# Kernel optimization log

Hardware: AMD Instinct MI355X
Metric: run time of the kernel (lower is better)

The kernel has to match this reference:

```python
import jax, jax.numpy as jnp
import numpy as np

B, C, FS, Z_DIM, OUT_C, F_SIZE = 256, 512, 16, 64, 1, 3
NZ = FS * FS  # 256


def setup_inputs() -> dict:
    key = jax.random.key(0)
    k1, k2, k3, k4, k5 = jax.random.split(key, 5)
    # z: [B, C, H, W]
    z = jax.random.normal(k1, (B, C, FS, FS), dtype=jnp.float32)
    # 512 independent per-channel Linear(Nz -> z_dim): stacked weights/biases
    lim_in = 1.0 / np.sqrt(NZ)
    W_in = jax.random.uniform(k2, (C, NZ, Z_DIM), minval=-lim_in, maxval=lim_in, dtype=jnp.float32)
    b_in = jax.random.uniform(k3, (C, Z_DIM), minval=-lim_in, maxval=lim_in, dtype=jnp.float32)
    # shared Linear(z_dim -> out_channels*f_size*f_size)
    lim_out = 1.0 / np.sqrt(Z_DIM)
    W_out = jax.random.uniform(k4, (Z_DIM, OUT_C * F_SIZE * F_SIZE), minval=-lim_out, maxval=lim_out, dtype=jnp.float32)
    b_out = jax.random.uniform(k5, (OUT_C * F_SIZE * F_SIZE,), minval=-lim_out, maxval=lim_out, dtype=jnp.float32)
    return {"z": z, "W_in": W_in, "b_in": b_in, "W_out": W_out, "b_out": b_out}


def reference(z, W_in, b_in, W_out, b_out):
    batch = z.shape[0]
    # flatten each channel's HxW map: [B, C, Nz]
    x = z.reshape(batch, C, NZ)
    # per-channel Linear as one batched GEMM: [B, C, z_dim]
    a = jnp.einsum('bcn,cnz->bcz', x, W_in) + b_in[None, :, :]
    # shared output Linear: [B, C, out_c*f*f]
    k = jnp.einsum('bcz,zk->bck', a, W_out) + b_out
    # [B, C, out_channels, f_size, f_size]
    return k.reshape(batch, C, OUT_C, F_SIZE, F_SIZE)
```

## Files before the change

### kernel.cpp

```cpp
#include <hip/hip_runtime.h>

#define BB 256
#define CC 512
#define NZ 256
#define ZD 64
#define KK 9
#define WFSZ (KK * NZ)

template<int CTRL>
__device__ __forceinline__ float dpp_add(float v) {
    int o = __builtin_amdgcn_update_dpp(0, __float_as_int(v), CTRL, 0xF, 0xF, true);
    return v + __int_as_float(o);
}
__device__ __forceinline__ float red8(float v) {
    v = dpp_add<0xB1>(v);
    v = dpp_add<0x4E>(v);
    v = dpp_add<0x141>(v);
    return v;
}

__global__ __launch_bounds__(512, 2)
void wf_kernel(const float* __restrict__ W_in, const float* __restrict__ b_in,
               const float* __restrict__ W_out, const float* __restrict__ b_out,
               float* __restrict__ wf, float* __restrict__ biask) {
    __shared__ __align__(16) float s_woutT[KK * ZD];
    __shared__ float s_bin[ZD];
    const int c = blockIdx.x;
    const int t = threadIdx.x;

    for (int i = t; i < KK * ZD; i += 512) {
        float v = W_out[i];
        int zz = i / KK, k = i - zz * KK;
        s_woutT[k * ZD + zz] = v;
    }
    if (t < ZD) s_bin[t] = b_in[c * ZD + t];
    __syncthreads();

    const int n = t >> 1, half = t & 1;
    const float* wrow = W_in + ((size_t)c * NZ + n) * ZD + half * 32;
    float acc[KK];
#pragma unroll
    for (int k = 0; k < KK; ++k) acc[k] = 0.f;
#pragma unroll
    for (int j = 0; j < 8; ++j) {
        const float4 w = *reinterpret_cast<const float4*>(wrow + 4 * j);
#pragma unroll
        for (int k = 0; k < KK; ++k) {
            const float4 wo = *reinterpret_cast<const float4*>(
                &s_woutT[k * ZD + half * 32 + 4 * j]);
            acc[k] += w.x * wo.x + w.y * wo.y + w.z * wo.z + w.w * wo.w;
        }
    }
#pragma unroll
    for (int k = 0; k < KK; ++k) acc[k] = dpp_add<0xB1>(acc[k]);
    if (half == 0) {
#pragma unroll
        for (int k = 0; k < KK; ++k)
            wf[(size_t)c * WFSZ + k * NZ + n] = acc[k];
    }
    if (t < KK) {
        float s = 0.f;
        for (int zz = 0; zz < ZD; ++zz) s += s_bin[zz] * s_woutT[t * ZD + zz];
        biask[c * KK + t] = s + b_out[t];
    }
}

__global__ __launch_bounds__(256, 2)
void out_kernel(const float* __restrict__ z, const float* __restrict__ wf,
                const float* __restrict__ biask, float* __restrict__ out) {
    __shared__ __align__(16) float s_wf[WFSZ];
    __shared__ float s_bias[KK];

    const int cid = blockIdx.x & (CC - 1);
    const int chunk = blockIdx.x >> 9;
    const int t = threadIdx.x;
    const int lane = t & 63;
    const int wave = t >> 6;
    const int g = lane >> 3;
    const int sub = lane & 7;
    const int b0 = chunk * 64 + wave * 16 + g * 2;

    const size_t bstr = (size_t)CC * NZ;
    const float* xp = z + ((size_t)b0 * CC + cid) * NZ + sub * 4;
    float4 x0[8], x1[8];
#pragma unroll
    for (int j = 0; j < 8; ++j)
        x0[j] = *reinterpret_cast<const float4*>(xp + j * 32);
#pragma unroll
    for (int j = 0; j < 8; ++j)
        x1[j] = *reinterpret_cast<const float4*>(xp + bstr + j * 32);

    {
        const float4* wfg = reinterpret_cast<const float4*>(wf + (size_t)cid * WFSZ);
        float4* s4 = reinterpret_cast<float4*>(s_wf);
        for (int i = t; i < WFSZ / 4; i += 256) s4[i] = wfg[i];
        if (t < KK) s_bias[t] = biask[cid * KK + t];
    }
    __syncthreads();

    float a0[KK], a1[KK];
#pragma unroll
    for (int k = 0; k < KK; ++k) { a0[k] = 0.f; a1[k] = 0.f; }
#pragma unroll
    for (int k = 0; k < KK; ++k) {
#pragma unroll
        for (int j = 0; j < 8; ++j) {
            const float4 wfv = *reinterpret_cast<const float4*>(
                &s_wf[k * NZ + sub * 4 + j * 32]);
            a0[k] += x0[j].x * wfv.x + x0[j].y * wfv.y + x0[j].z * wfv.z + x0[j].w * wfv.w;
            a1[k] += x1[j].x * wfv.x + x1[j].y * wfv.y + x1[j].z * wfv.z + x1[j].w * wfv.w;
        }
    }
#pragma unroll
    for (int k = 0; k < KK; ++k) { a0[k] = red8(a0[k]); a1[k] = red8(a1[k]); }

    const float biasS = s_bias[sub];
    float v0 = a0[0], v1 = a1[0];
#pragma unroll
    for (int k = 1; k < 8; ++k) {
        if (sub == k) { v0 = a0[k]; v1 = a1[k]; }
    }
    const size_t o0 = ((size_t)b0 * CC + cid) * KK;
    const size_t o1 = o0 + (size_t)CC * KK;
    out[o0 + sub] = v0 + biasS;
    out[o1 + sub] = v1 + biasS;
    if (sub == 0) {
        out[o0 + 8] = a0[8] + s_bias[8];
        out[o1 + 8] = a1[8] + s_bias[8];
    }
}

extern "C" void kernel_launch(void* const* d_in, const int* in_sizes, int n_in,
                              void* d_out, int out_size, void* d_ws, size_t ws_size,
                              hipStream_t stream) {
    const float* z     = (const float*)d_in[0];
    const float* W_in  = (const float*)d_in[1];
    const float* b_in  = (const float*)d_in[2];
    const float* W_out = (const float*)d_in[3];
    const float* b_out = (const float*)d_in[4];
    float* out = (float*)d_out;

    float* wf    = (float*)d_ws;
    float* biask = (float*)d_ws + (size_t)CC * WFSZ;

    wf_kernel<<<dim3(CC), dim3(512), 0, stream>>>(W_in, b_in, W_out, b_out, wf, biask);
    out_kernel<<<dim3(4 * CC), dim3(256), 0, stream>>>(z, wf, biask, out);
}
```

Before: 233.9 us.

## Stream z through double-buffered LDS tiles, one block per channel

The output kernel now launches one block per channel instead of four batch chunks per channel. Each block loops over the batch in tiles of 32 rows and prefetches the next z tile into a second LDS buffer with asynchronous global-to-LDS loads while the current tile is being computed. The fused weight slice is loaded into LDS once per channel instead of four times, and the reduction widens to 16 lanes. In exchange the grid shrinks to 512 blocks with about 73KB of LDS each, which lowers parallelism. Correctness also depends on the async LDS loads having completed before each barrier.

Measured after the change: 228.8 us. -2.2%, faster.

```diff
diff --git a/kernel.cpp b/kernel.cpp
--- a/kernel.cpp
+++ b/kernel.cpp
@@ -6,17 +6,27 @@
 #define ZD 64
 #define KK 9
 #define WFSZ (KK * NZ)
+#define TR 32
+#define NT (BB / TR)
 
 template<int CTRL>
 __device__ __forceinline__ float dpp_add(float v) {
     int o = __builtin_amdgcn_update_dpp(0, __float_as_int(v), CTRL, 0xF, 0xF, true);
     return v + __int_as_float(o);
 }
-__device__ __forceinline__ float red8(float v) {
+__device__ __forceinline__ float red16(float v) {
     v = dpp_add<0xB1>(v);
     v = dpp_add<0x4E>(v);
     v = dpp_add<0x141>(v);
+    v = dpp_add<0x140>(v);
     return v;
+}
+
+__device__ __forceinline__ void gld_lds16(const float* g, float* l) {
+    __builtin_amdgcn_global_load_lds(
+        (const __attribute__((address_space(1))) unsigned int*)(g),
+        (__attribute__((address_space(3))) unsigned int*)(l),
+        16, 0, 0);
 }
 
 __global__ __launch_bounds__(512, 2)
@@ -68,65 +78,78 @@
 __global__ __launch_bounds__(256, 2)
 void out_kernel(const float* __restrict__ z, const float* __restrict__ wf,
                 const float* __restrict__ biask, float* __restrict__ out) {
+    __shared__ __align__(16) float s_z[2][TR * NZ];
     __shared__ __align__(16) float s_wf[WFSZ];
-    __shared__ float s_bias[KK];
+    __shared__ float s_b[KK];
 
-    const int cid = blockIdx.x & (CC - 1);
-    const int chunk = blockIdx.x >> 9;
+    const int c = blockIdx.x;
     const int t = threadIdx.x;
     const int lane = t & 63;
     const int wave = t >> 6;
-    const int g = lane >> 3;
-    const int sub = lane & 7;
-    const int b0 = chunk * 64 + wave * 16 + g * 2;
+    const int g16 = lane >> 4;
+    const int s16 = lane & 15;
 
-    const size_t bstr = (size_t)CC * NZ;
-    const float* xp = z + ((size_t)b0 * CC + cid) * NZ + sub * 4;
-    float4 x0[8], x1[8];
+    const size_t zrow = (size_t)CC * NZ;
+    const float* zc = z + (size_t)c * NZ;
+
 #pragma unroll
-    for (int j = 0; j < 8; ++j)
-        x0[j] = *reinterpret_cast<const float4*>(xp + j * 32);
-#pragma unroll
-    for (int j = 0; j < 8; ++j)
-        x1[j] = *reinterpret_cast<const float4*>(xp + bstr + j * 32);
+    for (int r = 0; r < 8; ++r)
+        gld_lds16(zc + (size_t)(wave * 8 + r) * zrow + lane * 4,
+                  &s_z[0][(wave * 8 + r) * NZ]);
 
     {
-        const float4* wfg = reinterpret_cast<const float4*>(wf + (size_t)cid * WFSZ);
+        const float4* g4 = reinterpret_cast<const float4*>(wf + (size_t)c * WFSZ);
         float4* s4 = reinterpret_cast<float4*>(s_wf);
-        for (int i = t; i < WFSZ / 4; i += 256) s4[i] = wfg[i];
-        if (t < KK) s_bias[t] = biask[cid * KK + t];
+        for (int i = t; i < WFSZ / 4; i += 256) s4[i] = g4[i];
+        if (t < KK) s_b[t] = biask[c * KK + t];
     }
-    __syncthreads();
 
-    float a0[KK], a1[KK];
+    const int r0 = wave * 8 + g16 * 2;
+
+#pragma unroll 1
+    for (int tl = 0; tl < NT; ++tl) {
+        __syncthreads();
+        const int cur = tl & 1;
+        if (tl + 1 < NT) {
+            const float* g0 = zc + (size_t)((tl + 1) * TR + wave * 8) * zrow;
 #pragma unroll
-    for (int k = 0; k < KK; ++k) { a0[k] = 0.f; a1[k] = 0.f; }
+            for (int r = 0; r < 8; ++r)
+                gld_lds16(g0 + (size_t)r * zrow + lane * 4,
+                          &s_z[cur ^ 1][(wave * 8 + r) * NZ]);
+        }
+
+        float a0[KK], a1[KK];
 #pragma unroll
-    for (int k = 0; k < KK; ++k) {
+        for (int k = 0; k < KK; ++k) { a0[k] = 0.f; a1[k] = 0.f; }
 #pragma unroll
-        for (int j = 0; j < 8; ++j) {
-            const float4 wfv = *reinterpret_cast<const float4*>(
-                &s_wf[k * NZ + sub * 4 + j * 32]);
-            a0[k] += x0[j].x * wfv.x + x0[j].y * wfv.y + x0[j].z * wfv.z + x0[j].w * wfv.w;
-            a1[k] += x1[j].x * wfv.x + x1[j].y * wfv.y + x1[j].z * wfv.z + x1[j].w * wfv.w;
+        for (int j = 0; j < 4; ++j) {
+            const float4 x0 = *reinterpret_cast<const float4*>(
+                &s_z[cur][r0 * NZ + j * 64 + s16 * 4]);
+            const float4 x1 = *reinterpret_cast<const float4*>(
+                &s_z[cur][(r0 + 1) * NZ + j * 64 + s16 * 4]);
+#pragma unroll
+            for (int k = 0; k < KK; ++k) {
+                const float4 w = *reinterpret_cast<const float4*>(
+                    &s_wf[k * NZ + j * 64 + s16 * 4]);
+                a0[k] += x0.x * w.x + x0.y * w.y + x0.z * w.z + x0.w * w.w;
+                a1[k] += x1.x * w.x + x1.y * w.y + x1.z * w.z + x1.w * w.w;
+            }
         }
-    }
 #pragma unroll
-    for (int k = 0; k < KK; ++k) { a0[k] = red8(a0[k]); a1[k] = red8(a1[k]); }
+        for (int k = 0; k < KK; ++k) { a0[k] = red16(a0[k]); a1[k] = red16(a1[k]); }
 
-    const float biasS = s_bias[sub];
-    float v0 = a0[0], v1 = a1[0];
+        float v0 = a0[0], v1 = a1[0];
 #pragma unroll
-    for (int k = 1; k < 8; ++k) {
-        if (sub == k) { v0 = a0[k]; v1 = a1[k]; }
-    }
-    const size_t o0 = ((size_t)b0 * CC + cid) * KK;
-    const size_t o1 = o0 + (size_t)CC * KK;
-    out[o0 + sub] = v0 + biasS;
-    out[o1 + sub] = v1 + biasS;
-    if (sub == 0) {
-        out[o0 + 8] = a0[8] + s_bias[8];
-        out[o1 + 8] = a1[8] + s_bias[8];
+        for (int k = 1; k < KK; ++k) {
+            if (s16 == k) { v0 = a0[k]; v1 = a1[k]; }
+        }
+        if (s16 < KK) {
+            const float bk = s_b[s16];
+            const int b = tl * TR + r0;
+            const size_t o0 = ((size_t)b * CC + c) * KK;
+            out[o0 + s16] = v0 + bk;
+            out[o0 + (size_t)CC * KK + s16] = v1 + bk;
+        }
     }
 }
 
@@ -140,9 +163,9 @@
     const float* b_out = (const float*)d_in[4];
     float* out = (float*)d_out;
 
-    float* wf    = (float*)d_ws;
+    float* wfbuf = (float*)d_ws;
     float* biask = (float*)d_ws + (size_t)CC * WFSZ;
 
-    wf_kernel<<<dim3(CC), dim3(512), 0, stream>>>(W_in, b_in, W_out, b_out, wf, biask);
-    out_kernel<<<dim3(4 * CC), dim3(256), 0, stream>>>(z, wf, biask, out);
+    wf_kernel<<<dim3(CC), dim3(512), 0, stream>>>(W_in, b_in, W_out, b_out, wfbuf, biask);
+    out_kernel<<<dim3(CC), dim3(256), 0, stream>>>(z, wfbuf, biask, out);
 }
```

## Store fused weights as bf16 and read them directly from global without LDS

Applied to the files above, without the earlier changes.

The fused per-channel weight matrix (W_in·W_out) is written in bf16 rather than fp32, which halves the workspace traffic. The output kernel drops LDS staging and the block barrier, re-maps blocks to cover 2 batches by 32 channels, and reads the bf16 weights straight from global/L2. It loops over channels with 16-lane groups and a 16-wide DPP reduction, and raises occupancy to 6 blocks per CU. Rounding the fused weights to bf16 adds precision error, and each weight row is now re-read per batch pair through cache instead of being shared via LDS.

Measured after the change: 243.4 us. 4.1% more time.

```diff
diff --git a/kernel.cpp b/kernel.cpp
--- a/kernel.cpp
+++ b/kernel.cpp
@@ -12,17 +12,27 @@
     int o = __builtin_amdgcn_update_dpp(0, __float_as_int(v), CTRL, 0xF, 0xF, true);
     return v + __int_as_float(o);
 }
-__device__ __forceinline__ float red8(float v) {
+__device__ __forceinline__ float red16(float v) {
     v = dpp_add<0xB1>(v);
     v = dpp_add<0x4E>(v);
     v = dpp_add<0x141>(v);
+    v = dpp_add<0x140>(v);
     return v;
+}
+
+__device__ __forceinline__ unsigned short f2bf(float f) {
+    unsigned u = __float_as_uint(f);
+    u += 0x7FFF + ((u >> 16) & 1);
+    return (unsigned short)(u >> 16);
+}
+__device__ __forceinline__ float bf2f(unsigned short h) {
+    return __uint_as_float((unsigned)h << 16);
 }
 
 __global__ __launch_bounds__(512, 2)
 void wf_kernel(const float* __restrict__ W_in, const float* __restrict__ b_in,
                const float* __restrict__ W_out, const float* __restrict__ b_out,
-               float* __restrict__ wf, float* __restrict__ biask) {
+               unsigned short* __restrict__ wfb, float* __restrict__ biask) {
     __shared__ __align__(16) float s_woutT[KK * ZD];
     __shared__ float s_bin[ZD];
     const int c = blockIdx.x;
@@ -56,7 +66,7 @@
     if (half == 0) {
 #pragma unroll
         for (int k = 0; k < KK; ++k)
-            wf[(size_t)c * WFSZ + k * NZ + n] = acc[k];
+            wfb[((size_t)c * KK + k) * NZ + n] = f2bf(acc[k]);
     }
     if (t < KK) {
         float s = 0.f;
@@ -65,68 +75,59 @@
     }
 }
 
-__global__ __launch_bounds__(256, 2)
-void out_kernel(const float* __restrict__ z, const float* __restrict__ wf,
+__global__ __launch_bounds__(256, 6)
+void out_kernel(const float* __restrict__ z, const unsigned short* __restrict__ wfb,
                 const float* __restrict__ biask, float* __restrict__ out) {
-    __shared__ __align__(16) float s_wf[WFSZ];
-    __shared__ float s_bias[KK];
+    const int bid = blockIdx.x;
+    const int b0 = (bid >> 4) * 2;
+    const int cbase = (bid & 15) * 32;
 
-    const int cid = blockIdx.x & (CC - 1);
-    const int chunk = blockIdx.x >> 9;
     const int t = threadIdx.x;
+    const int wave = t >> 6;
     const int lane = t & 63;
-    const int wave = t >> 6;
-    const int g = lane >> 3;
-    const int sub = lane & 7;
-    const int b0 = chunk * 64 + wave * 16 + g * 2;
+    const int g = lane >> 4;
+    const int s16 = lane & 15;
 
-    const size_t bstr = (size_t)CC * NZ;
-    const float* xp = z + ((size_t)b0 * CC + cid) * NZ + sub * 4;
-    float4 x0[8], x1[8];
+    const int b = b0 + (g & 1);
+    const int cofs = g >> 1;
+
+#pragma unroll 1
+    for (int s = 0; s < 4; ++s) {
+        const int c = cbase + wave * 8 + s * 2 + cofs;
+        const float* zr = z + ((size_t)b * CC + c) * NZ + s16 * 4;
+
+        float4 x[4];
 #pragma unroll
-    for (int j = 0; j < 8; ++j)
-        x0[j] = *reinterpret_cast<const float4*>(xp + j * 32);
+        for (int j = 0; j < 4; ++j)
+            x[j] = *reinterpret_cast<const float4*>(zr + j * 64);
+
+        const unsigned short* wr = wfb + (size_t)c * WFSZ + s16 * 4;
+        float a[KK];
 #pragma unroll
-    for (int j = 0; j < 8; ++j)
-        x1[j] = *reinterpret_cast<const float4*>(xp + bstr + j * 32);
+        for (int k = 0; k < KK; ++k) {
+            float acc = 0.f;
+#pragma unroll
+            for (int j = 0; j < 4; ++j) {
+                const ushort4 w4 = *reinterpret_cast<const ushort4*>(
+                    wr + k * NZ + j * 64);
+                acc += x[j].x * bf2f(w4.x) + x[j].y * bf2f(w4.y)
+                     + x[j].z * bf2f(w4.z) + x[j].w * bf2f(w4.w);
+            }
+            a[k] = acc;
+        }
 
-    {
-        const float4* wfg = reinterpret_cast<const float4*>(wf + (size_t)cid * WFSZ);
-        float4* s4 = reinterpret_cast<float4*>(s_wf);
-        for (int i = t; i < WFSZ / 4; i += 256) s4[i] = wfg[i];
-        if (t < KK) s_bias[t] = biask[cid * KK + t];
-    }
-    __syncthreads();
+#pragma unroll
+        for (int k = 0; k < KK; ++k) a[k] = red16(a[k]);
 
-    float a0[KK], a1[KK];
+        float v = a[0];
 #pragma unroll
-    for (int k = 0; k < KK; ++k) { a0[k] = 0.f; a1[k] = 0.f; }
-#pragma unroll
-    for (int k = 0; k < KK; ++k) {
-#pragma unroll
-        for (int j = 0; j < 8; ++j) {
-            const float4 wfv = *reinterpret_cast<const float4*>(
-                &s_wf[k * NZ + sub * 4 + j * 32]);
-            a0[k] += x0[j].x * wfv.x + x0[j].y * wfv.y + x0[j].z * wfv.z + x0[j].w * wfv.w;
-            a1[k] += x1[j].x * wfv.x + x1[j].y * wfv.y + x1[j].z * wfv.z + x1[j].w * wfv.w;
+        for (int k = 1; k < KK; ++k) {
+            if (s16 == k) v = a[k];
         }
-    }
-#pragma unroll
-    for (int k = 0; k < KK; ++k) { a0[k] = red8(a0[k]); a1[k] = red8(a1[k]); }
-
-    const float biasS = s_bias[sub];
-    float v0 = a0[0], v1 = a1[0];
-#pragma unroll
-    for (int k = 1; k < 8; ++k) {
-        if (sub == k) { v0 = a0[k]; v1 = a1[k]; }
-    }
-    const size_t o0 = ((size_t)b0 * CC + cid) * KK;
-    const size_t o1 = o0 + (size_t)CC * KK;
-    out[o0 + sub] = v0 + biasS;
-    out[o1 + sub] = v1 + biasS;
-    if (sub == 0) {
-        out[o0 + 8] = a0[8] + s_bias[8];
-        out[o1 + 8] = a1[8] + s_bias[8];
+        if (s16 < KK) {
+            v += biask[c * KK + s16];
+            out[((size_t)b * CC + c) * KK + s16] = v;
+        }
     }
 }
 
@@ -140,9 +141,9 @@
     const float* b_out = (const float*)d_in[4];
     float* out = (float*)d_out;
 
-    float* wf    = (float*)d_ws;
-    float* biask = (float*)d_ws + (size_t)CC * WFSZ;
+    unsigned short* wfb = (unsigned short*)d_ws;
+    float* biask = (float*)((char*)d_ws + (size_t)CC * WFSZ * 2);
 
-    wf_kernel<<<dim3(CC), dim3(512), 0, stream>>>(W_in, b_in, W_out, b_out, wf, biask);
-    out_kernel<<<dim3(4 * CC), dim3(256), 0, stream>>>(z, wf, biask, out);
+    wf_kernel<<<dim3(CC), dim3(512), 0, stream>>>(W_in, b_in, W_out, b_out, wfb, biask);
+    out_kernel<<<dim3(2048), dim3(256), 0, stream>>>(z, wfb, biask, out);
 }
```
